# Optimization experiments

Hardware: AMD Instinct MI355X
Metric: run time of the kernel (lower is better)

The kernel has to match this reference:

```python
import jax, jax.numpy as jnp
import numpy as np

# Config constants (mirror Qwen3_5TextConfig)
H = 1024        # hidden_size
I = 512         # moe_intermediate_size
IS = 2048       # shared_expert_intermediate_size
E = 16          # num_experts
TOP_K = 4       # num_experts_per_tok
NORM_TOPK = True
B, S = 1, 1024


def setup_inputs() -> dict:
    key = jax.random.key(0)
    ks = jax.random.split(key, 10)
    s = 0.02
    return {
        "hidden_states": jax.random.normal(ks[0], (B, S, H), jnp.float32),
        "w_router": (jax.random.normal(ks[1], (H, E), jnp.float32) * s),
        # stacked expert weights; Linear(H->I) stored as [E, H, I] for einsum
        "w_gate": (jax.random.normal(ks[2], (E, H, I), jnp.float32) * s),
        "w_up": (jax.random.normal(ks[3], (E, H, I), jnp.float32) * s),
        "w_down": (jax.random.normal(ks[4], (E, I, H), jnp.float32) * s),
        # shared expert (dense MLP)
        "ws_gate": (jax.random.normal(ks[5], (H, IS), jnp.float32) * s),
        "ws_up": (jax.random.normal(ks[6], (H, IS), jnp.float32) * s),
        "ws_down": (jax.random.normal(ks[7], (IS, H), jnp.float32) * s),
        "w_shared_gate": (jax.random.normal(ks[8], (H, 1), jnp.float32) * s),
    }


def reference(hidden_states, w_router, w_gate, w_up, w_down,
              ws_gate, ws_up, ws_down, w_shared_gate):
    b, sl, hd = hidden_states.shape
    x = hidden_states.reshape(-1, hd)              # [T, H]
    T = x.shape[0]

    # --- router: softmax in fp32, top-k, optional renormalization ---
    router_logits = x @ w_router                   # [T, E]
    probs = jax.nn.softmax(router_logits.astype(jnp.float32), axis=-1)
    top_w, top_i = jax.lax.top_k(probs, TOP_K)     # [T, K]
    if NORM_TOPK:
        top_w = top_w / top_w.sum(axis=-1, keepdims=True)
    # dense per-token expert weights (zeros off the top-k)
    dense_w = jnp.zeros((T, E), x.dtype).at[jnp.arange(T)[:, None], top_i].set(
        top_w.astype(x.dtype))                     # [T, E]

    # --- expert MLPs (SwiGLU), computed for all experts then masked-combined ---
    g = jnp.einsum('th,ehi->tei', x, w_gate)       # [T, E, I]
    u = jnp.einsum('th,ehi->tei', x, w_up)         # [T, E, I]
    expert_out = jnp.einsum('tei,eih->teh', jax.nn.silu(g) * u, w_down)  # [T, E, H]
    moe_out = jnp.einsum('te,teh->th', dense_w, expert_out)             # [T, H]

    # --- shared expert + sigmoid gate ---
    shared = (jax.nn.silu(x @ ws_gate) * (x @ ws_up)) @ ws_down          # [T, H]
    shared_gate = jax.nn.sigmoid(x @ w_shared_gate)                      # [T, 1]
    out = (moe_out + shared_gate * shared).reshape(b, sl, hd)
    return out, router_logits
```

## Files before the change

### kernel.cpp

```cpp
#include <hip/hip_runtime.h>
#include <hip/hip_bf16.h>

#define T_ 1024
#define H_ 1024
#define I_ 512
#define IS_ 2048
#define E_ 16

typedef __attribute__((ext_vector_type(8))) short short8;
typedef __attribute__((ext_vector_type(4))) float f32x4;

__device__ __forceinline__ unsigned short f2bf(float f) {
  unsigned u = __builtin_bit_cast(unsigned, f);
  unsigned r = (u + 0x7fffu + ((u >> 16) & 1u)) >> 16;
  return (unsigned short)r;
}

__device__ __forceinline__ void gload16(const void* g, void* l) {
  __builtin_amdgcn_global_load_lds(
      (const __attribute__((address_space(1))) unsigned int*)g,
      (__attribute__((address_space(3))) unsigned int*)l, 16, 0, 0);
}

__device__ __forceinline__ void transpose_cstrip(
    const float* __restrict__ src, unsigned short* __restrict__ dst,
    int C, int Rf, int r_start, int n0, int nch) {
  __shared__ unsigned short tile[2][64 * 66];
  int tid = threadIdx.x;
  int c = (tid & 15) << 2;
  int r0 = (tid >> 4) << 2;
  int orr = tid >> 2;
  int ks = (tid & 3) << 4;
  const float* sp0 = src + (long)(r_start + r0) * C + n0 + c;
  unsigned short* dbase = dst + (long)(n0 + orr) * Rf + r_start + ks;

  float4 va[4], vb[4];
#pragma unroll
  for (int r = 0; r < 4; r++) va[r] = *(const float4*)(sp0 + (long)r * C);

  for (int t = 0; t < nch; t += 2) {
    {
      const float* sp = sp0 + (long)(t + 1) * 64 * C;
#pragma unroll
      for (int r = 0; r < 4; r++) vb[r] = *(const float4*)(sp + (long)r * C);
    }
    {
      unsigned short* tb = &tile[0][0];
      ushort4 w;
      w = (ushort4){f2bf(va[0].x), f2bf(va[1].x), f2bf(va[2].x), f2bf(va[3].x)};
      *(ushort4*)&tb[(c + 0) * 66 + r0] = w;
      w = (ushort4){f2bf(va[0].y), f2bf(va[1].y), f2bf(va[2].y), f2bf(va[3].y)};
      *(ushort4*)&tb[(c + 1) * 66 + r0] = w;
      w = (ushort4){f2bf(va[0].z), f2bf(va[1].z), f2bf(va[2].z), f2bf(va[3].z)};
      *(ushort4*)&tb[(c + 2) * 66 + r0] = w;
      w = (ushort4){f2bf(va[0].w), f2bf(va[1].w), f2bf(va[2].w), f2bf(va[3].w)};
      *(ushort4*)&tb[(c + 3) * 66 + r0] = w;
      asm volatile("s_waitcnt lgkmcnt(0)" ::: "memory");
      __builtin_amdgcn_sched_barrier(0);
      __builtin_amdgcn_s_barrier();
      __builtin_amdgcn_sched_barrier(0);
      uint4 o0 = *(const uint4*)&tb[orr * 66 + ks];
      uint4 o1 = *(const uint4*)&tb[orr * 66 + ks + 8];
      unsigned short* d = dbase + (long)t * 64;
      *(uint4*)d = o0;
      *(uint4*)(d + 8) = o1;
    }
    if (t + 2 < nch) {
      const float* sp = sp0 + (long)(t + 2) * 64 * C;
#pragma unroll
      for (int r = 0; r < 4; r++) va[r] = *(const float4*)(sp + (long)r * C);
    }
    {
      unsigned short* tb = &tile[1][0];
      ushort4 w;
      w = (ushort4){f2bf(vb[0].x), f2bf(vb[1].x), f2bf(vb[2].x), f2bf(vb[3].x)};
      *(ushort4*)&tb[(c + 0) * 66 + r0] = w;
      w = (ushort4){f2bf(vb[0].y), f2bf(vb[1].y), f2bf(vb[2].y), f2bf(vb[3].y)};
      *(ushort4*)&tb[(c + 1) * 66 + r0] = w;
      w = (ushort4){f2bf(vb[0].z), f2bf(vb[1].z), f2bf(vb[2].z), f2bf(vb[3].z)};
      *(ushort4*)&tb[(c + 2) * 66 + r0] = w;
      w = (ushort4){f2bf(vb[0].w), f2bf(vb[1].w), f2bf(vb[2].w), f2bf(vb[3].w)};
      *(ushort4*)&tb[(c + 3) * 66 + r0] = w;
      asm volatile("s_waitcnt lgkmcnt(0)" ::: "memory");
      __builtin_amdgcn_sched_barrier(0);
      __builtin_amdgcn_s_barrier();
      __builtin_amdgcn_sched_barrier(0);
      uint4 o0 = *(const uint4*)&tb[orr * 66 + ks];
      uint4 o1 = *(const uint4*)&tb[orr * 66 + ks + 8];
      unsigned short* d = dbase + (long)(t + 1) * 64;
      *(uint4*)d = o0;
      *(uint4*)(d + 8) = o1;
    }
  }
}

__global__ __launch_bounds__(256) void k_router(
    const float* __restrict__ x, const float* __restrict__ wr,
    const float* __restrict__ wshg,
    unsigned short* __restrict__ xb, float* __restrict__ logits_out,
    int* __restrict__ top_i, float* __restrict__ top_w,
    float* __restrict__ gate_sig) {
  __shared__ float red[4][17];
  int t = blockIdx.x, tid = threadIdx.x;
  int h0 = tid << 2;
  float acc[17];
#pragma unroll
  for (int e = 0; e < 17; e++) acc[e] = 0.f;
  float4 xv = *(const float4*)(x + (long)t * H_ + h0);
  float4 wsh = *(const float4*)(wshg + h0);
  ushort4 xo;
  xo.x = f2bf(xv.x); xo.y = f2bf(xv.y); xo.z = f2bf(xv.z); xo.w = f2bf(xv.w);
  *(ushort4*)(xb + (long)t * H_ + h0) = xo;
  float xs[4] = {xv.x, xv.y, xv.z, xv.w};
  float ws[4] = {wsh.x, wsh.y, wsh.z, wsh.w};
#pragma unroll
  for (int j = 0; j < 4; j++) {
    const float4* w4 = (const float4*)(wr + (long)(h0 + j) * 16);
    float4 w0 = w4[0], w1 = w4[1], w2 = w4[2], w3 = w4[3];
    float xvj = xs[j];
    acc[0] += xvj * w0.x; acc[1] += xvj * w0.y; acc[2] += xvj * w0.z; acc[3] += xvj * w0.w;
    acc[4] += xvj * w1.x; acc[5] += xvj * w1.y; acc[6] += xvj * w1.z; acc[7] += xvj * w1.w;
    acc[8] += xvj * w2.x; acc[9] += xvj * w2.y; acc[10] += xvj * w2.z; acc[11] += xvj * w2.w;
    acc[12] += xvj * w3.x; acc[13] += xvj * w3.y; acc[14] += xvj * w3.z; acc[15] += xvj * w3.w;
    acc[16] += xvj * ws[j];
  }
#pragma unroll
  for (int off = 32; off >= 1; off >>= 1) {
#pragma unroll
    for (int e = 0; e < 17; e++) acc[e] += __shfl_xor(acc[e], off, 64);
  }
  int wid = tid >> 6, lane = tid & 63;
  if (lane == 0) {
#pragma unroll
    for (int e = 0; e < 17; e++) red[wid][e] = acc[e];
  }
  __syncthreads();
  if (tid == 0) {
    float a[17];
#pragma unroll
    for (int e = 0; e < 17; e++)
      a[e] = red[0][e] + red[1][e] + red[2][e] + red[3][e];
    float m = a[0];
#pragma unroll
    for (int e = 1; e < 16; e++) m = fmaxf(m, a[e]);
    float p[16], s = 0.f;
#pragma unroll
    for (int e = 0; e < 16; e++) { p[e] = expf(a[e] - m); s += p[e]; }
    float inv = 1.f / s;
#pragma unroll
    for (int e = 0; e < 16; e++) p[e] *= inv;
    int ti[4]; float tw[4]; float tsum = 0.f;
#pragma unroll
    for (int k = 0; k < 4; k++) {
      float best = -1.f; int bi = 0;
#pragma unroll
      for (int e = 0; e < 16; e++)
        if (p[e] > best) { best = p[e]; bi = e; }
      ti[k] = bi; tw[k] = best; tsum += best; p[bi] = -2.f;
    }
    float rn = 1.f / tsum;
#pragma unroll
    for (int e = 0; e < 16; e++) logits_out[(long)t * 16 + e] = a[e];
#pragma unroll
    for (int k = 0; k < 4; k++) {
      top_i[t * 4 + k] = ti[k];
      top_w[t * 4 + k] = tw[k] * rn;
    }
    gate_sig[t] = 1.f / (1.f + expf(-a[16]));
  }
}

__global__ __launch_bounds__(256) void k_wtb(
    const float* __restrict__ wg, const float* __restrict__ wu,
    const float* __restrict__ wd, const float* __restrict__ wsg,
    const float* __restrict__ wsu, const float* __restrict__ wsd,
    unsigned short* __restrict__ WGUT, unsigned short* __restrict__ WDT,
    unsigned short* __restrict__ WSGUT, unsigned short* __restrict__ WSDT,
    const int* __restrict__ top_i, const float* __restrict__ top_w,
    int* __restrict__ counts, int* __restrict__ offsets,
    int* __restrict__ perm, float* __restrict__ wslot,
    int* __restrict__ gu_tiles, int* __restrict__ dn_tiles,
    int* __restrict__ ntl) {
  int id = blockIdx.x;
  if (id < 960) {
    const float* src; unsigned short* dst; int C, Rf, r0s, n0, nch;
    if (id < 64) {
      int s = id >> 2, q = id & 3;
      src = wsd; dst = WSDT; C = H_; Rf = IS_;
      n0 = s * 64; r0s = q * 512; nch = 8;
    } else if (id < 128) {
      int l = id - 64, s = l >> 1, h = l & 1;
      src = wsg; dst = WSGUT; C = IS_; Rf = H_;
      n0 = s * 64; r0s = h * 512; nch = 8;
    } else if (id < 192) {
      int l = id - 128, s = l >> 1, h = l & 1;
      src = wsu; dst = WSGUT + (long)IS_ * H_; C = IS_; Rf = H_;
      n0 = s * 64; r0s = h * 512; nch = 8;
    } else if (id < 448) {
      int l = id - 192, e = l >> 4, s = (l >> 1) & 7, h = l & 1;
      src = wg + (long)e * H_ * I_; dst = WGUT + (long)e * 2 * I_ * H_;
      C = I_; Rf = H_; n0 = s * 64; r0s = h * 512; nch = 8;
    } else if (id < 704) {
      int l = id - 448, e = l >> 4, s = (l >> 1) & 7, h = l & 1;
      src = wu + (long)e * H_ * I_;
      dst = WGUT + (long)e * 2 * I_ * H_ + (long)I_ * H_;
      C = I_; Rf = H_; n0 = s * 64; r0s = h * 512; nch = 8;
    } else {
      int l = id - 704, e = l >> 4, s = l & 15;
      src = wd + (long)e * I_ * H_; dst = WDT + (long)e * H_ * I_;
      C = H_; Rf = I_; n0 = s * 64; r0s = 0; nch = 8;
    }
    transpose_cstrip(src, dst, C, Rf, r0s, n0, nch);
    return;
  }
  __shared__ int cnt[E_], cur[E_], mt[E_], pg[E_];
  int tid = threadIdx.x;
  if (tid < E_) cnt[tid] = 0;
  __syncthreads();
  for (int i = tid; i < T_ * 4; i += 256)
    atomicAdd(&cnt[top_i[i]], 1);
  __syncthreads();
  if (tid == 0) {
    int run = 0, trun = 0;
    for (int e = 0; e < E_; e++) {
      int c = cnt[e];
      counts[e] = c;
      offsets[e] = run;
      cur[e] = run;
      run += c;
      mt[e] = (c + 63) >> 6;
      pg[e] = trun;
      trun += mt[e];
    }
    ntl[0] = 512 + trun * 8;
    ntl[1] = 256 + trun * 16;
  }
  __syncthreads();
  for (int i = tid; i < T_ * 4; i += 256) {
    int e = top_i[i];
    int pos = atomicAdd(&cur[e], 1);
    perm[pos] = i >> 2;
    wslot[pos] = top_w[i];
  }
  for (int i = tid; i < 512; i += 256)
    gu_tiles[i] = ((i >> 5) << 6) | (i & 31);
  if (tid < 256)
    dn_tiles[tid] = ((tid >> 4) << 6) | (tid & 15);
  int trun = pg[E_ - 1] + mt[E_ - 1];
  for (int i = tid; i < trun * 8; i += 256) {
    int m = i >> 3, x = i & 7;
    int e = 0;
    while (e < E_ - 1 && m >= pg[e] + mt[e]) e++;
    int y = m - pg[e];
    gu_tiles[512 + i] = ((e + 1) << 12) | (y << 6) | x;
  }
  for (int i = tid; i < trun * 16; i += 256) {
    int m = i >> 4, x = i & 15;
    int e = 0;
    while (e < E_ - 1 && m >= pg[e] + mt[e]) e++;
    int y = m - pg[e];
    dn_tiles[256 + i] = ((e + 1) << 12) | (y << 6) | x;
  }
}

__global__ __launch_bounds__(256) void k_gemm_gu(
    const unsigned short* __restrict__ XB,
    const unsigned short* __restrict__ WSGUT, const unsigned short* __restrict__ WGUT,
    unsigned short* __restrict__ HSB, unsigned short* __restrict__ HB,
    const int* __restrict__ counts, const int* __restrict__ offsets,
    const int* __restrict__ perm, const int* __restrict__ gu_tiles,
    const int* __restrict__ ntl) {
  __shared__ unsigned short lds[3][6144];

  int tid = threadIdx.x, wid = tid >> 6, lane = tid & 63;
  int sub = lane >> 2;
  int ksw = ((lane & 3) ^ ((sub >> 1) & 3)) << 3;
  int soff = wid * 512;
  int fr = lane & 15, quad = lane >> 4;
  int fslot = (quad ^ ((fr >> 1) & 3)) << 3;
  int wm = (wid >> 1) * 32, wn = (wid & 1) * 32;

  int n_tiles = ntl[0];
  for (int w = blockIdx.x; w < n_tiles; w += gridDim.x) {
    int twd = gu_tiles[w];
    int z = twd >> 12;
    int mtile = ((twd >> 6) & 63) * 64;
    int ntile = (twd & 63) * 64;
    int M, row_base, uoff, ldd;
    const unsigned short* B0;
    unsigned short* DST;
    const int* pp;
    if (z == 0) {
      M = T_; row_base = 0; B0 = WSGUT; uoff = IS_;
      DST = HSB; ldd = IS_; pp = nullptr;
    } else {
      int e = z - 1;
      M = counts[e];
      row_base = offsets[e];
      B0 = WGUT + (long)e * 2 * I_ * H_;
      uoff = I_;
      DST = HB; ldd = I_; pp = perm;
    }

    int rm = mtile + wid * 16 + sub;
    if (rm > M - 1) rm = M - 1;
    long arow = pp ? (long)pp[row_base + rm] : (long)(row_base + rm);
    const unsigned short* aptr = XB + arow * H_ + ksw;
    int rbn = ntile + wid * 16 + sub;
    const unsigned short* bgptr = B0 + (long)rbn * H_ + ksw;
    const unsigned short* buptr = B0 + (long)(rbn + uoff) * H_ + ksw;

    f32x4 acc[2][2][2];
#pragma unroll
    for (int h = 0; h < 2; h++)
#pragma unroll
      for (int i = 0; i < 2; i++)
#pragma unroll
        for (int j = 0; j < 2; j++) acc[h][i][j] = (f32x4){0.f, 0.f, 0.f, 0.f};

    auto STAGE = [&](int slot, int kt) {
      int ko = kt * 32;
      unsigned short* base = &lds[slot][0];
      gload16(aptr + ko, base + soff);
      gload16(bgptr + ko, base + 2048 + soff);
      gload16(buptr + ko, base + 4096 + soff);
    };

    const int NK = H_ / 32;
    asm volatile("s_waitcnt lgkmcnt(0)" ::: "memory");
    __builtin_amdgcn_s_barrier();
    __builtin_amdgcn_sched_barrier(0);
    STAGE(0, 0);
    STAGE(1, 1);
    int cur = 0, stg = 2;
    for (int kt = 0; kt < NK; kt++) {
      if (kt + 1 < NK) asm volatile("s_waitcnt vmcnt(3)" ::: "memory");
      else             asm volatile("s_waitcnt vmcnt(0)" ::: "memory");
      __builtin_amdgcn_s_barrier();
      __builtin_amdgcn_sched_barrier(0);
      if (kt + 2 < NK) STAGE(stg, kt + 2);
      __builtin_amdgcn_sched_barrier(0);
      const unsigned short* As = &lds[cur][0];
      const unsigned short* Bg = &lds[cur][2048];
      const unsigned short* Bu = &lds[cur][4096];
      short8 af[2], bg[2], bu[2];
#pragma unroll
      for (int i = 0; i < 2; i++)
        af[i] = *(const short8*)(&As[(wm + i * 16 + fr) * 32 + fslot]);
#pragma unroll
      for (int j = 0; j < 2; j++) {
        bg[j] = *(const short8*)(&Bg[(wn + j * 16 + fr) * 32 + fslot]);
        bu[j] = *(const short8*)(&Bu[(wn + j * 16 + fr) * 32 + fslot]);
      }
#pragma unroll
      for (int i = 0; i < 2; i++)
#pragma unroll
        for (int j = 0; j < 2; j++) {
          acc[0][i][j] = __builtin_amdgcn_mfma_f32_16x16x32_bf16(af[i], bg[j], acc[0][i][j], 0, 0, 0);
          acc[1][i][j] = __builtin_amdgcn_mfma_f32_16x16x32_bf16(af[i], bu[j], acc[1][i][j], 0, 0, 0);
        }
      asm volatile("s_waitcnt lgkmcnt(0)" ::: "memory");
      __builtin_amdgcn_sched_barrier(0);
      cur = (cur == 2) ? 0 : cur + 1;
      stg = (stg == 2) ? 0 : stg + 1;
    }

#pragma unroll
    for (int i = 0; i < 2; i++) {
      int m0 = mtile + wm + i * 16 + quad * 4;
#pragma unroll
      for (int j = 0; j < 2; j++) {
        int col = ntile + wn + j * 16 + fr;
#pragma unroll
        for (int r = 0; r < 4; r++) {
          int m = m0 + r;
          if (m < M) {
            float g = acc[0][i][j][r], u = acc[1][i][j][r];
            DST[(long)(row_base + m) * ldd + col] = f2bf(g / (1.f + expf(-g)) * u);
          }
        }
      }
    }
  }
}

__global__ __launch_bounds__(256) void k_gemm_dn(
    const unsigned short* __restrict__ HSB, const unsigned short* __restrict__ WSDT,
    const unsigned short* __restrict__ HB, const unsigned short* __restrict__ WDT,
    const int* __restrict__ counts, const int* __restrict__ offsets,
    const int* __restrict__ perm, const float* __restrict__ wslot,
    const float* __restrict__ gate_sig,
    const int* __restrict__ dn_tiles, const int* __restrict__ ntl,
    float* __restrict__ out) {
  __shared__ unsigned short lds[3][4096];

  int tid = threadIdx.x, wid = tid >> 6, lane = tid & 63;
  int sub = lane >> 2;
  int ksw = ((lane & 3) ^ ((sub >> 1) & 3)) << 3;
  int soff = wid * 512;
  int fr = lane & 15, quad = lane >> 4;
  int fslot = (quad ^ ((fr >> 1) & 3)) << 3;
  int wm = (wid >> 1) * 32, wn = (wid & 1) * 32;

  int n_tiles = ntl[1];
  for (int w = blockIdx.x; w < n_tiles; w += gridDim.x) {
    int twd = dn_tiles[w];
    int z = twd >> 12;
    int mtile = ((twd >> 6) & 63) * 64;
    int ntile = (twd & 63) * 64;
    const unsigned short *A, *B;
    int K, M, rb;
    if (z == 0) {
      A = HSB; K = IS_; M = T_; rb = 0; B = WSDT;
    } else {
      int e = z - 1;
      M = counts[e];
      rb = offsets[e];
      A = HB; K = I_; B = WDT + (long)e * H_ * I_;
    }

    int rm = mtile + wid * 16 + sub;
    if (rm > M - 1) rm = M - 1;
    const unsigned short* aptr = A + (long)(rb + rm) * K + ksw;
    int rbn = ntile + wid * 16 + sub;
    const unsigned short* bptr = B + (long)rbn * K + ksw;

    f32x4 acc[2][2];
#pragma unroll
    for (int i = 0; i < 2; i++)
#pragma unroll
      for (int j = 0; j < 2; j++) acc[i][j] = (f32x4){0.f, 0.f, 0.f, 0.f};

    auto STAGE = [&](int slot, int kt) {
      int ko = kt * 32;
      unsigned short* base = &lds[slot][0];
      gload16(aptr + ko, base + soff);
      gload16(bptr + ko, base + 2048 + soff);
    };

    const int NK = K / 32;
    asm volatile("s_waitcnt lgkmcnt(0)" ::: "memory");
    __builtin_amdgcn_s_barrier();
    __builtin_amdgcn_sched_barrier(0);
    STAGE(0, 0);
    STAGE(1, 1);
    int cur = 0, stg = 2;
    for (int kt = 0; kt < NK; kt++) {
      if (kt + 1 < NK) asm volatile("s_waitcnt vmcnt(2)" ::: "memory");
      else             asm volatile("s_waitcnt vmcnt(0)" ::: "memory");
      __builtin_amdgcn_s_barrier();
      __builtin_amdgcn_sched_barrier(0);
      if (kt + 2 < NK) STAGE(stg, kt + 2);
      __builtin_amdgcn_sched_barrier(0);
      const unsigned short* As = &lds[cur][0];
      const unsigned short* Bs = &lds[cur][2048];
      short8 af[2], bf[2];
#pragma unroll
      for (int i = 0; i < 2; i++)
        af[i] = *(const short8*)(&As[(wm + i * 16 + fr) * 32 + fslot]);
#pragma unroll
      for (int j = 0; j < 2; j++)
        bf[j] = *(const short8*)(&Bs[(wn + j * 16 + fr) * 32 + fslot]);
#pragma unroll
      for (int i = 0; i < 2; i++)
#pragma unroll
        for (int j = 0; j < 2; j++)
          acc[i][j] = __builtin_amdgcn_mfma_f32_16x16x32_bf16(af[i], bf[j], acc[i][j], 0, 0, 0);
      asm volatile("s_waitcnt lgkmcnt(0)" ::: "memory");
      __builtin_amdgcn_sched_barrier(0);
      cur = (cur == 2) ? 0 : cur + 1;
      stg = (stg == 2) ? 0 : stg + 1;
    }

#pragma unroll
    for (int i = 0; i < 2; i++) {
      int m0 = mtile + wm + i * 16 + quad * 4;
#pragma unroll
      for (int j = 0; j < 2; j++) {
        int col = ntile + wn + j * 16 + fr;
#pragma unroll
        for (int r = 0; r < 4; r++) {
          int m = m0 + r;
          if (m < M) {
            if (z == 0) {
              float gs = gate_sig[m];
              atomicAdd(&out[(long)m * H_ + col], gs * acc[i][j][r]);
            } else {
              int tkn = perm[rb + m];
              float wgt = wslot[rb + m];
              atomicAdd(&out[(long)tkn * H_ + col], wgt * acc[i][j][r]);
            }
          }
        }
      }
    }
  }
}

extern "C" void kernel_launch(void* const* d_in, const int* in_sizes, int n_in,
                              void* d_out, int out_size, void* d_ws, size_t ws_size,
                              hipStream_t stream) {
  const float* x    = (const float*)d_in[0];
  const float* wrt  = (const float*)d_in[1];
  const float* wg   = (const float*)d_in[2];
  const float* wu   = (const float*)d_in[3];
  const float* wd   = (const float*)d_in[4];
  const float* wsg  = (const float*)d_in[5];
  const float* wsu  = (const float*)d_in[6];
  const float* wsd  = (const float*)d_in[7];
  const float* wshg = (const float*)d_in[8];
  float* out = (float*)d_out;
  float* logits_out = out + (long)T_ * H_;

  char* ws = (char*)d_ws;
  size_t off = 0;
  auto take = [&](size_t bytes) -> void* {
    void* p = ws + off;
    off += (bytes + 255) & ~(size_t)255;
    return p;
  };

  unsigned short* XB    = (unsigned short*)take((size_t)T_ * H_ * 2);
  unsigned short* WGUT  = (unsigned short*)take((size_t)E_ * 2 * I_ * H_ * 2);
  unsigned short* WDT   = (unsigned short*)take((size_t)E_ * H_ * I_ * 2);
  unsigned short* WSGUT = (unsigned short*)take((size_t)2 * IS_ * H_ * 2);
  unsigned short* WSDT  = (unsigned short*)take((size_t)H_ * IS_ * 2);
  unsigned short* HSB   = (unsigned short*)take((size_t)T_ * IS_ * 2);
  unsigned short* HB    = (unsigned short*)take((size_t)4096 * I_ * 2);
  int*   counts   = (int*)take(64);
  int*   offsets  = (int*)take(64);
  int*   top_i    = (int*)take((size_t)T_ * 4 * 4);
  float* top_w    = (float*)take((size_t)T_ * 4 * 4);
  int*   perm     = (int*)take((size_t)4096 * 4);
  float* wslot    = (float*)take((size_t)4096 * 4);
  float* gate_sig = (float*)take((size_t)T_ * 4);
  int*   gu_tiles = (int*)take((size_t)2048 * 4);
  int*   dn_tiles = (int*)take((size_t)2048 * 4);
  int*   ntl      = (int*)take(64);

  k_router<<<T_, 256, 0, stream>>>(x, wrt, wshg, XB, logits_out,
                                   top_i, top_w, gate_sig);
  k_wtb<<<961, 256, 0, stream>>>(wg, wu, wd, wsg, wsu, wsd,
                                 WGUT, WDT, WSGUT, WSDT,
                                 top_i, top_w, counts, offsets, perm, wslot,
                                 gu_tiles, dn_tiles, ntl);
  k_gemm_gu<<<1024, 256, 0, stream>>>(XB, WSGUT, WGUT, HSB, HB,
                                      counts, offsets, perm, gu_tiles, ntl);
  k_gemm_dn<<<1280, 256, 0, stream>>>(HSB, WSDT, HB, WDT,
                                      counts, offsets, perm, wslot, gate_sig,
                                      dn_tiles, ntl, out);
}
```

Baseline: 264.9 us.

## Fuse fp32 weight conversion into GEMM loads, drop separate transpose kernel

Removes the standalone kernel that transposed and converted all expert and shared weights to bf16. The GEMM kernels now read fp32 weights directly, convert them to bf16 in registers, and write them transposed into padded LDS with register double-buffering. This avoids a full extra pass over the weights and the bf16 round trip through global memory. In exchange, each GEMM tile re-reads and re-converts fp32 weights (twice the bytes, and weights are shared by several M tiles), and the async global-to-LDS loads give way to strided scalar loads.

```diff
diff --git a/kernel.cpp b/kernel.cpp
--- a/kernel.cpp
+++ b/kernel.cpp
@@ -16,82 +16,8 @@
   return (unsigned short)r;
 }
 
-__device__ __forceinline__ void gload16(const void* g, void* l) {
-  __builtin_amdgcn_global_load_lds(
-      (const __attribute__((address_space(1))) unsigned int*)g,
-      (__attribute__((address_space(3))) unsigned int*)l, 16, 0, 0);
-}
-
-__device__ __forceinline__ void transpose_cstrip(
-    const float* __restrict__ src, unsigned short* __restrict__ dst,
-    int C, int Rf, int r_start, int n0, int nch) {
-  __shared__ unsigned short tile[2][64 * 66];
-  int tid = threadIdx.x;
-  int c = (tid & 15) << 2;
-  int r0 = (tid >> 4) << 2;
-  int orr = tid >> 2;
-  int ks = (tid & 3) << 4;
-  const float* sp0 = src + (long)(r_start + r0) * C + n0 + c;
-  unsigned short* dbase = dst + (long)(n0 + orr) * Rf + r_start + ks;
-
-  float4 va[4], vb[4];
-#pragma unroll
-  for (int r = 0; r < 4; r++) va[r] = *(const float4*)(sp0 + (long)r * C);
-
-  for (int t = 0; t < nch; t += 2) {
-    {
-      const float* sp = sp0 + (long)(t + 1) * 64 * C;
-#pragma unroll
-      for (int r = 0; r < 4; r++) vb[r] = *(const float4*)(sp + (long)r * C);
-    }
-    {
-      unsigned short* tb = &tile[0][0];
-      ushort4 w;
-      w = (ushort4){f2bf(va[0].x), f2bf(va[1].x), f2bf(va[2].x), f2bf(va[3].x)};
-      *(ushort4*)&tb[(c + 0) * 66 + r0] = w;
-      w = (ushort4){f2bf(va[0].y), f2bf(va[1].y), f2bf(va[2].y), f2bf(va[3].y)};
-      *(ushort4*)&tb[(c + 1) * 66 + r0] = w;
-      w = (ushort4){f2bf(va[0].z), f2bf(va[1].z), f2bf(va[2].z), f2bf(va[3].z)};
-      *(ushort4*)&tb[(c + 2) * 66 + r0] = w;
-      w = (ushort4){f2bf(va[0].w), f2bf(va[1].w), f2bf(va[2].w), f2bf(va[3].w)};
-      *(ushort4*)&tb[(c + 3) * 66 + r0] = w;
-      asm volatile("s_waitcnt lgkmcnt(0)" ::: "memory");
-      __builtin_amdgcn_sched_barrier(0);
-      __builtin_amdgcn_s_barrier();
-      __builtin_amdgcn_sched_barrier(0);
-      uint4 o0 = *(const uint4*)&tb[orr * 66 + ks];
-      uint4 o1 = *(const uint4*)&tb[orr * 66 + ks + 8];
-      unsigned short* d = dbase + (long)t * 64;
-      *(uint4*)d = o0;
-      *(uint4*)(d + 8) = o1;
-    }
-    if (t + 2 < nch) {
-      const float* sp = sp0 + (long)(t + 2) * 64 * C;
-#pragma unroll
-      for (int r = 0; r < 4; r++) va[r] = *(const float4*)(sp + (long)r * C);
-    }
-    {
-      unsigned short* tb = &tile[1][0];
-      ushort4 w;
-      w = (ushort4){f2bf(vb[0].x), f2bf(vb[1].x), f2bf(vb[2].x), f2bf(vb[3].x)};
-      *(ushort4*)&tb[(c + 0) * 66 + r0] = w;
-      w = (ushort4){f2bf(vb[0].y), f2bf(vb[1].y), f2bf(vb[2].y), f2bf(vb[3].y)};
-      *(ushort4*)&tb[(c + 1) * 66 + r0] = w;
-      w = (ushort4){f2bf(vb[0].z), f2bf(vb[1].z), f2bf(vb[2].z), f2bf(vb[3].z)};
-      *(ushort4*)&tb[(c + 2) * 66 + r0] = w;
-      w = (ushort4){f2bf(vb[0].w), f2bf(vb[1].w), f2bf(vb[2].w), f2bf(vb[3].w)};
-      *(ushort4*)&tb[(c + 3) * 66 + r0] = w;
-      asm volatile("s_waitcnt lgkmcnt(0)" ::: "memory");
-      __builtin_amdgcn_sched_barrier(0);
-      __builtin_amdgcn_s_barrier();
-      __builtin_amdgcn_sched_barrier(0);
-      uint4 o0 = *(const uint4*)&tb[orr * 66 + ks];
-      uint4 o1 = *(const uint4*)&tb[orr * 66 + ks + 8];
-      unsigned short* d = dbase + (long)(t + 1) * 64;
-      *(uint4*)d = o0;
-      *(uint4*)(d + 8) = o1;
-    }
-  }
+__device__ __forceinline__ unsigned pk2(float lo, float hi) {
+  return (unsigned)f2bf(lo) | ((unsigned)f2bf(hi) << 16);
 }
 
 __global__ __launch_bounds__(256) void k_router(
@@ -170,49 +96,12 @@
   }
 }
 
-__global__ __launch_bounds__(256) void k_wtb(
-    const float* __restrict__ wg, const float* __restrict__ wu,
-    const float* __restrict__ wd, const float* __restrict__ wsg,
-    const float* __restrict__ wsu, const float* __restrict__ wsd,
-    unsigned short* __restrict__ WGUT, unsigned short* __restrict__ WDT,
-    unsigned short* __restrict__ WSGUT, unsigned short* __restrict__ WSDT,
+__global__ __launch_bounds__(256) void k_build(
     const int* __restrict__ top_i, const float* __restrict__ top_w,
     int* __restrict__ counts, int* __restrict__ offsets,
     int* __restrict__ perm, float* __restrict__ wslot,
     int* __restrict__ gu_tiles, int* __restrict__ dn_tiles,
     int* __restrict__ ntl) {
-  int id = blockIdx.x;
-  if (id < 960) {
-    const float* src; unsigned short* dst; int C, Rf, r0s, n0, nch;
-    if (id < 64) {
-      int s = id >> 2, q = id & 3;
-      src = wsd; dst = WSDT; C = H_; Rf = IS_;
-      n0 = s * 64; r0s = q * 512; nch = 8;
-    } else if (id < 128) {
-      int l = id - 64, s = l >> 1, h = l & 1;
-      src = wsg; dst = WSGUT; C = IS_; Rf = H_;
-      n0 = s * 64; r0s = h * 512; nch = 8;
-    } else if (id < 192) {
-      int l = id - 128, s = l >> 1, h = l & 1;
-      src = wsu; dst = WSGUT + (long)IS_ * H_; C = IS_; Rf = H_;
-      n0 = s * 64; r0s = h * 512; nch = 8;
-    } else if (id < 448) {
-      int l = id - 192, e = l >> 4, s = (l >> 1) & 7, h = l & 1;
-      src = wg + (long)e * H_ * I_; dst = WGUT + (long)e * 2 * I_ * H_;
-      C = I_; Rf = H_; n0 = s * 64; r0s = h * 512; nch = 8;
-    } else if (id < 704) {
-      int l = id - 448, e = l >> 4, s = (l >> 1) & 7, h = l & 1;
-      src = wu + (long)e * H_ * I_;
-      dst = WGUT + (long)e * 2 * I_ * H_ + (long)I_ * H_;
-      C = I_; Rf = H_; n0 = s * 64; r0s = h * 512; nch = 8;
-    } else {
-      int l = id - 704, e = l >> 4, s = l & 15;
-      src = wd + (long)e * I_ * H_; dst = WDT + (long)e * H_ * I_;
-      C = H_; Rf = I_; n0 = s * 64; r0s = 0; nch = 8;
-    }
-    transpose_cstrip(src, dst, C, Rf, r0s, n0, nch);
-    return;
-  }
   __shared__ int cnt[E_], cur[E_], mt[E_], pg[E_];
   int tid = threadIdx.x;
   if (tid < E_) cnt[tid] = 0;
@@ -248,37 +137,40 @@
     dn_tiles[tid] = ((tid >> 4) << 6) | (tid & 15);
   int trun = pg[E_ - 1] + mt[E_ - 1];
   for (int i = tid; i < trun * 8; i += 256) {
-    int m = i >> 3, x = i & 7;
+    int m = i >> 3, xx = i & 7;
     int e = 0;
     while (e < E_ - 1 && m >= pg[e] + mt[e]) e++;
     int y = m - pg[e];
-    gu_tiles[512 + i] = ((e + 1) << 12) | (y << 6) | x;
+    gu_tiles[512 + i] = ((e + 1) << 12) | (y << 6) | xx;
   }
   for (int i = tid; i < trun * 16; i += 256) {
-    int m = i >> 4, x = i & 15;
+    int m = i >> 4, xx = i & 15;
     int e = 0;
     while (e < E_ - 1 && m >= pg[e] + mt[e]) e++;
     int y = m - pg[e];
-    dn_tiles[256 + i] = ((e + 1) << 12) | (y << 6) | x;
-  }
-}
+    dn_tiles[256 + i] = ((e + 1) << 12) | (y << 6) | xx;
+  }
+}
+
 
 __global__ __launch_bounds__(256) void k_gemm_gu(
     const unsigned short* __restrict__ XB,
-    const unsigned short* __restrict__ WSGUT, const unsigned short* __restrict__ WGUT,
+    const float* __restrict__ wsg, const float* __restrict__ wsu,
+    const float* __restrict__ wg, const float* __restrict__ wu,
     unsigned short* __restrict__ HSB, unsigned short* __restrict__ HB,
     const int* __restrict__ counts, const int* __restrict__ offsets,
     const int* __restrict__ perm, const int* __restrict__ gu_tiles,
     const int* __restrict__ ntl) {
-  __shared__ unsigned short lds[3][6144];
+  __shared__ unsigned short lds[2][7680];
 
   int tid = threadIdx.x, wid = tid >> 6, lane = tid & 63;
-  int sub = lane >> 2;
-  int ksw = ((lane & 3) ^ ((sub >> 1) & 3)) << 3;
-  int soff = wid * 512;
   int fr = lane & 15, quad = lane >> 4;
-  int fslot = (quad ^ ((fr >> 1) & 3)) << 3;
+  int q8 = quad * 8;
   int wm = (wid >> 1) * 32, wn = (wid & 1) * 32;
+  int ar = tid >> 2, aj = tid & 3;
+  int awoff = ar * 40 + aj * 8;
+  int n_l = tid & 63, bq = tid >> 6;
+  int bwoff = n_l * 40 + bq * 8;
 
   int n_tiles = ntl[0];
   for (int w = blockIdx.x; w < n_tiles; w += gridDim.x) {
@@ -286,29 +178,29 @@
     int z = twd >> 12;
     int mtile = ((twd >> 6) & 63) * 64;
     int ntile = (twd & 63) * 64;
-    int M, row_base, uoff, ldd;
-    const unsigned short* B0;
+    int M, row_base, ldB, ldd;
+    const float *BG, *BU;
     unsigned short* DST;
     const int* pp;
     if (z == 0) {
-      M = T_; row_base = 0; B0 = WSGUT; uoff = IS_;
+      M = T_; row_base = 0; BG = wsg; BU = wsu; ldB = IS_;
       DST = HSB; ldd = IS_; pp = nullptr;
     } else {
       int e = z - 1;
       M = counts[e];
       row_base = offsets[e];
-      B0 = WGUT + (long)e * 2 * I_ * H_;
-      uoff = I_;
+      BG = wg + (long)e * H_ * I_;
+      BU = wu + (long)e * H_ * I_;
+      ldB = I_;
       DST = HB; ldd = I_; pp = perm;
     }
 
-    int rm = mtile + wid * 16 + sub;
+    int rm = mtile + ar;
     if (rm > M - 1) rm = M - 1;
     long arow = pp ? (long)pp[row_base + rm] : (long)(row_base + rm);
-    const unsigned short* aptr = XB + arow * H_ + ksw;
-    int rbn = ntile + wid * 16 + sub;
-    const unsigned short* bgptr = B0 + (long)rbn * H_ + ksw;
-    const unsigned short* buptr = B0 + (long)(rbn + uoff) * H_ + ksw;
+    const unsigned short* aptr = XB + arow * H_ + aj * 8;
+    const float* bgp = BG + (long)bq * 8 * ldB + ntile + n_l;
+    const float* bup = BU + (long)bq * 8 * ldB + ntile + n_l;
 
     f32x4 acc[2][2][2];
 #pragma unroll
@@ -318,51 +210,74 @@
 #pragma unroll
         for (int j = 0; j < 2; j++) acc[h][i][j] = (f32x4){0.f, 0.f, 0.f, 0.f};
 
-    auto STAGE = [&](int slot, int kt) {
-      int ko = kt * 32;
-      unsigned short* base = &lds[slot][0];
-      gload16(aptr + ko, base + soff);
-      gload16(bgptr + ko, base + 2048 + soff);
-      gload16(buptr + ko, base + 4096 + soff);
+    float vgA[8], vuA[8], vgB[8], vuB[8];
+    short8 avA, avB;
+
+    auto GLOAD = [&](float (&VG)[8], float (&VU)[8], short8& AV, int kt) {
+      long ko = (long)kt * 32 * ldB;
+#pragma unroll
+      for (int i = 0; i < 8; i++) {
+        VG[i] = bgp[ko + (long)i * ldB];
+        VU[i] = bup[ko + (long)i * ldB];
+      }
+      AV = *(const short8*)(aptr + kt * 32);
+    };
+    auto GWRITE = [&](float (&VG)[8], float (&VU)[8], short8& AV, int s) {
+      uint4 pg_, pu_;
+      pg_.x = pk2(VG[0], VG[1]); pg_.y = pk2(VG[2], VG[3]);
+      pg_.z = pk2(VG[4], VG[5]); pg_.w = pk2(VG[6], VG[7]);
+      pu_.x = pk2(VU[0], VU[1]); pu_.y = pk2(VU[2], VU[3]);
+      pu_.z = pk2(VU[4], VU[5]); pu_.w = pk2(VU[6], VU[7]);
+      *(short8*)&lds[s][awoff] = AV;
+      *(uint4*)&lds[s][2560 + bwoff] = pg_;
+      *(uint4*)&lds[s][5120 + bwoff] = pu_;
+    };
+    auto GCOMP = [&](int s) {
+      const unsigned short* L = &lds[s][0];
+      short8 af0 = *(const short8*)&L[(wm + fr) * 40 + q8];
+      short8 af1 = *(const short8*)&L[(wm + 16 + fr) * 40 + q8];
+      short8 bg0 = *(const short8*)&L[2560 + (wn + fr) * 40 + q8];
+      short8 bg1 = *(const short8*)&L[2560 + (wn + 16 + fr) * 40 + q8];
+      short8 bu0 = *(const short8*)&L[5120 + (wn + fr) * 40 + q8];
+      short8 bu1 = *(const short8*)&L[5120 + (wn + 16 + fr) * 40 + q8];
+      acc[0][0][0] = __builtin_amdgcn_mfma_f32_16x16x32_bf16(af0, bg0, acc[0][0][0], 0, 0, 0);
+      acc[0][0][1] = __builtin_amdgcn_mfma_f32_16x16x32_bf16(af0, bg1, acc[0][0][1], 0, 0, 0);
+      acc[0][1][0] = __builtin_amdgcn_mfma_f32_16x16x32_bf16(af1, bg0, acc[0][1][0], 0, 0, 0);
+      acc[0][1][1] = __builtin_amdgcn_mfma_f32_16x16x32_bf16(af1, bg1, acc[0][1][1], 0, 0, 0);
+      acc[1][0][0] = __builtin_amdgcn_mfma_f32_16x16x32_bf16(af0, bu0, acc[1][0][0], 0, 0, 0);
+      acc[1][0][1] = __builtin_amdgcn_mfma_f32_16x16x32_bf16(af0, bu1, acc[1][0][1], 0, 0, 0);
+      acc[1][1][0] = __builtin_amdgcn_mfma_f32_16x16x32_bf16(af1, bu0, acc[1][1][0], 0, 0, 0);
+      acc[1][1][1] = __builtin_amdgcn_mfma_f32_16x16x32_bf16(af1, bu1, acc[1][1][1], 0, 0, 0);
     };
 
     const int NK = H_ / 32;
     asm volatile("s_waitcnt lgkmcnt(0)" ::: "memory");
+    __builtin_amdgcn_sched_barrier(0);
     __builtin_amdgcn_s_barrier();
     __builtin_amdgcn_sched_barrier(0);
-    STAGE(0, 0);
-    STAGE(1, 1);
-    int cur = 0, stg = 2;
-    for (int kt = 0; kt < NK; kt++) {
-      if (kt + 1 < NK) asm volatile("s_waitcnt vmcnt(3)" ::: "memory");
-      else             asm volatile("s_waitcnt vmcnt(0)" ::: "memory");
+    GLOAD(vgA, vuA, avA, 0);
+    GLOAD(vgB, vuB, avB, 1);
+    GWRITE(vgA, vuA, avA, 0);
+    asm volatile("s_waitcnt lgkmcnt(0)" ::: "memory");
+    __builtin_amdgcn_sched_barrier(0);
+    __builtin_amdgcn_s_barrier();
+    __builtin_amdgcn_sched_barrier(0);
+#pragma unroll 1
+    for (int kt = 0; kt < NK; kt += 2) {
+      if (kt + 2 < NK) GLOAD(vgA, vuA, avA, kt + 2);
+      GWRITE(vgB, vuB, avB, 1);
+      GCOMP(0);
+      asm volatile("s_waitcnt lgkmcnt(0)" ::: "memory");
+      __builtin_amdgcn_sched_barrier(0);
       __builtin_amdgcn_s_barrier();
       __builtin_amdgcn_sched_barrier(0);
-      if (kt + 2 < NK) STAGE(stg, kt + 2);
-      __builtin_amdgcn_sched_barrier(0);
-      const unsigned short* As = &lds[cur][0];
-      const unsigned short* Bg = &lds[cur][2048];
-      const unsigned short* Bu = &lds[cur][4096];
-      short8 af[2], bg[2], bu[2];
-#pragma unroll
-      for (int i = 0; i < 2; i++)
-        af[i] = *(const short8*)(&As[(wm + i * 16 + fr) * 32 + fslot]);
-#pragma unroll
-      for (int j = 0; j < 2; j++) {
-        bg[j] = *(const short8*)(&Bg[(wn + j * 16 + fr) * 32 + fslot]);
-        bu[j] = *(const short8*)(&Bu[(wn + j * 16 + fr) * 32 + fslot]);
-      }
-#pragma unroll
-      for (int i = 0; i < 2; i++)
-#pragma unroll
-        for (int j = 0; j < 2; j++) {
-          acc[0][i][j] = __builtin_amdgcn_mfma_f32_16x16x32_bf16(af[i], bg[j], acc[0][i][j], 0, 0, 0);
-          acc[1][i][j] = __builtin_amdgcn_mfma_f32_16x16x32_bf16(af[i], bu[j], acc[1][i][j], 0, 0, 0);
-        }
+      if (kt + 3 < NK) GLOAD(vgB, vuB, avB, kt + 3);
+      if (kt + 2 < NK) GWRITE(vgA, vuA, avA, 0);
+      GCOMP(1);
       asm volatile("s_waitcnt lgkmcnt(0)" ::: "memory");
       __builtin_amdgcn_sched_barrier(0);
-      cur = (cur == 2) ? 0 : cur + 1;
-      stg = (stg == 2) ? 0 : stg + 1;
+      __builtin_amdgcn_s_barrier();
+      __builtin_amdgcn_sched_barrier(0);
     }
 
 #pragma unroll
@@ -385,22 +300,23 @@
 }
 
 __global__ __launch_bounds__(256) void k_gemm_dn(
-    const unsigned short* __restrict__ HSB, const unsigned short* __restrict__ WSDT,
-    const unsigned short* __restrict__ HB, const unsigned short* __restrict__ WDT,
+    const unsigned short* __restrict__ HSB, const float* __restrict__ wsd,
+    const unsigned short* __restrict__ HB, const float* __restrict__ wd,
     const int* __restrict__ counts, const int* __restrict__ offsets,
     const int* __restrict__ perm, const float* __restrict__ wslot,
     const float* __restrict__ gate_sig,
     const int* __restrict__ dn_tiles, const int* __restrict__ ntl,
     float* __restrict__ out) {
-  __shared__ unsigned short lds[3][4096];
+  __shared__ unsigned short lds[2][5120];
 
   int tid = threadIdx.x, wid = tid >> 6, lane = tid & 63;
-  int sub = lane >> 2;
-  int ksw = ((lane & 3) ^ ((sub >> 1) & 3)) << 3;
-  int soff = wid * 512;
   int fr = lane & 15, quad = lane >> 4;
-  int fslot = (quad ^ ((fr >> 1) & 3)) << 3;
+  int q8 = quad * 8;
   int wm = (wid >> 1) * 32, wn = (wid & 1) * 32;
+  int ar = tid >> 2, aj = tid & 3;
+  int awoff = ar * 40 + aj * 8;
+  int n_l = tid & 63, bq = tid >> 6;
+  int bwoff = n_l * 40 + bq * 8;
 
   int n_tiles = ntl[1];
   for (int w = blockIdx.x; w < n_tiles; w += gridDim.x) {
@@ -408,22 +324,22 @@
     int z = twd >> 12;
     int mtile = ((twd >> 6) & 63) * 64;
     int ntile = (twd & 63) * 64;
-    const unsigned short *A, *B;
+    const unsigned short* A;
+    const float* B;
     int K, M, rb;
     if (z == 0) {
-      A = HSB; K = IS_; M = T_; rb = 0; B = WSDT;
+      A = HSB; K = IS_; M = T_; rb = 0; B = wsd;
     } else {
       int e = z - 1;
       M = counts[e];
       rb = offsets[e];
-      A = HB; K = I_; B = WDT + (long)e * H_ * I_;
-    }
-
-    int rm = mtile + wid * 16 + sub;
+      A = HB; K = I_; B = wd + (long)e * I_ * H_;
+    }
+
+    int rm = mtile + ar;
     if (rm > M - 1) rm = M - 1;
-    const unsigned short* aptr = A + (long)(rb + rm) * K + ksw;
-    int rbn = ntile + wid * 16 + sub;
-    const unsigned short* bptr = B + (long)rbn * K + ksw;
+    const unsigned short* aptr = A + (long)(rb + rm) * K + aj * 8;
+    const float* bp = B + (long)bq * 8 * H_ + ntile + n_l;
 
     f32x4 acc[2][2];
 #pragma unroll
@@ -431,45 +347,62 @@
 #pragma unroll
       for (int j = 0; j < 2; j++) acc[i][j] = (f32x4){0.f, 0.f, 0.f, 0.f};
 
-    auto STAGE = [&](int slot, int kt) {
-      int ko = kt * 32;
-      unsigned short* base = &lds[slot][0];
-      gload16(aptr + ko, base + soff);
-      gload16(bptr + ko, base + 2048 + soff);
+    float vA[8], vB[8];
+    short8 avA, avB;
+
+    auto DLOAD = [&](float (&V)[8], short8& AV, int kt) {
+      long ko = (long)kt * 32 * H_;
+#pragma unroll
+      for (int i = 0; i < 8; i++) V[i] = bp[ko + (long)i * H_];
+      AV = *(const short8*)(aptr + kt * 32);
+    };
+    auto DWRITE = [&](float (&V)[8], short8& AV, int s) {
+      uint4 pb_;
+      pb_.x = pk2(V[0], V[1]); pb_.y = pk2(V[2], V[3]);
+      pb_.z = pk2(V[4], V[5]); pb_.w = pk2(V[6], V[7]);
+      *(short8*)&lds[s][awoff] = AV;
+      *(uint4*)&lds[s][2560 + bwoff] = pb_;
+    };
+    auto DCOMP = [&](int s) {
+      const unsigned short* L = &lds[s][0];
+      short8 af0 = *(const short8*)&L[(wm + fr) * 40 + q8];
+      short8 af1 = *(const short8*)&L[(wm + 16 + fr) * 40 + q8];
+      short8 bf0 = *(const short8*)&L[2560 + (wn + fr) * 40 + q8];
+      short8 bf1 = *(const short8*)&L[2560 + (wn + 16 + fr) * 40 + q8];
+      acc[0][0] = __builtin_amdgcn_mfma_f32_16x16x32_bf16(af0, bf0, acc[0][0], 0, 0, 0);
+      acc[0][1] = __builtin_amdgcn_mfma_f32_16x16x32_bf16(af0, bf1, acc[0][1], 0, 0, 0);
+      acc[1][0] = __builtin_amdgcn_mfma_f32_16x16x32_bf16(af1, bf0, acc[1][0], 0, 0, 0);
+      acc[1][1] = __builtin_amdgcn_mfma_f32_16x16x32_bf16(af1, bf1, acc[1][1], 0, 0, 0);
     };
 
     const int NK = K / 32;
     asm volatile("s_waitcnt lgkmcnt(0)" ::: "memory");
+    __builtin_amdgcn_sched_barrier(0);
     __builtin_amdgcn_s_barrier();
     __builtin_amdgcn_sched_barrier(0);
-    STAGE(0, 0);
-    STAGE(1, 1);
-    int cur = 0, stg = 2;
-    for (int kt = 0; kt < NK; kt++) {
-      if (kt + 1 < NK) asm volatile("s_waitcnt vmcnt(2)" ::: "memory");
-      else             asm volatile("s_waitcnt vmcnt(0)" ::: "memory");
+    DLOAD(vA, avA, 0);
+    DLOAD(vB, avB, 1);
+    DWRITE(vA, avA, 0);
+    asm volatile("s_waitcnt lgkmcnt(0)" ::: "memory");
+    __builtin_amdgcn_sched_barrier(0);
+    __builtin_amdgcn_s_barrier();
+    __builtin_amdgcn_sched_barrier(0);
+#pragma unroll 1
+    for (int kt = 0; kt < NK; kt += 2) {
+      if (kt + 2 < NK) DLOAD(vA, avA, kt + 2);
+      DWRITE(vB, avB, 1);
+      DCOMP(0);
+      asm volatile("s_waitcnt lgkmcnt(0)" ::: "memory");
+      __builtin_amdgcn_sched_barrier(0);
       __builtin_amdgcn_s_barrier();
       __builtin_amdgcn_sched_barrier(0);
-      if (kt + 2 < NK) STAGE(stg, kt + 2);
-      __builtin_amdgcn_sched_barrier(0);
-      const unsigned short* As = &lds[cur][0];
-      const unsigned short* Bs = &lds[cur][2048];
-      short8 af[2], bf[2];
-#pragma unroll
-      for (int i = 0; i < 2; i++)
-        af[i] = *(const short8*)(&As[(wm + i * 16 + fr) * 32 + fslot]);
-#pragma unroll
-      for (int j = 0; j < 2; j++)
-        bf[j] = *(const short8*)(&Bs[(wn + j * 16 + fr) * 32 + fslot]);
-#pragma unroll
-      for (int i = 0; i < 2; i++)
-#pragma unroll
-        for (int j = 0; j < 2; j++)
-          acc[i][j] = __builtin_amdgcn_mfma_f32_16x16x32_bf16(af[i], bf[j], acc[i][j], 0, 0, 0);
+      if (kt + 3 < NK) DLOAD(vB, avB, kt + 3);
+      if (kt + 2 < NK) DWRITE(vA, avA, 0);
+      DCOMP(1);
       asm volatile("s_waitcnt lgkmcnt(0)" ::: "memory");
       __builtin_amdgcn_sched_barrier(0);
-      cur = (cur == 2) ? 0 : cur + 1;
-      stg = (stg == 2) ? 0 : stg + 1;
+      __builtin_amdgcn_s_barrier();
+      __builtin_amdgcn_sched_barrier(0);
     }
 
 #pragma unroll
@@ -521,10 +454,6 @@
   };
 
   unsigned short* XB    = (unsigned short*)take((size_t)T_ * H_ * 2);
-  unsigned short* WGUT  = (unsigned short*)take((size_t)E_ * 2 * I_ * H_ * 2);
-  unsigned short* WDT   = (unsigned short*)take((size_t)E_ * H_ * I_ * 2);
-  unsigned short* WSGUT = (unsigned short*)take((size_t)2 * IS_ * H_ * 2);
-  unsigned short* WSDT  = (unsigned short*)take((size_t)H_ * IS_ * 2);
   unsigned short* HSB   = (unsigned short*)take((size_t)T_ * IS_ * 2);
   unsigned short* HB    = (unsigned short*)take((size_t)4096 * I_ * 2);
   int*   counts   = (int*)take(64);
@@ -540,13 +469,11 @@
 
   k_router<<<T_, 256, 0, stream>>>(x, wrt, wshg, XB, logits_out,
                                    top_i, top_w, gate_sig);
-  k_wtb<<<961, 256, 0, stream>>>(wg, wu, wd, wsg, wsu, wsd,
-                                 WGUT, WDT, WSGUT, WSDT,
-                                 top_i, top_w, counts, offsets, perm, wslot,
+  k_build<<<1, 256, 0, stream>>>(top_i, top_w, counts, offsets, perm, wslot,
                                  gu_tiles, dn_tiles, ntl);
-  k_gemm_gu<<<1024, 256, 0, stream>>>(XB, WSGUT, WGUT, HSB, HB,
+  k_gemm_gu<<<1024, 256, 0, stream>>>(XB, wsg, wsu, wg, wu, HSB, HB,
                                       counts, offsets, perm, gu_tiles, ntl);
-  k_gemm_dn<<<1280, 256, 0, stream>>>(HSB, WSDT, HB, WDT,
+  k_gemm_dn<<<1280, 256, 0, stream>>>(HSB, wsd, HB, wd,
                                       counts, offsets, perm, wslot, gate_sig,
                                       dn_tiles, ntl, out);
 }
```

Result: slower. 313.4 us (+18.3%).
